# Optimization experiments

Hardware: AMD Instinct MI355X
Metric: run time of the kernel (lower is better)

The kernel has to match this reference:

```python
import jax, jax.numpy as jnp
import numpy as np

NUM_CLASSES = 14
IGNORE = 0
MAX_SAMPLES = 28 * 50
MAX_VIEWS = 50
TEMP = 0.1
THRESH = 0.3


def setup_inputs() -> dict:
    key = jax.random.key(0)
    B, Fd, D, H, W = 2, 128, 16, 128, 128
    N = B * D * H * W
    feats = jax.random.normal(key, (B, Fd, D, H, W), jnp.float32)
    idx = np.arange(N)
    pred = (idx % NUM_CLASSES).astype(np.int32)
    # alternate blocks: easy (label==pred) / hard (label!=pred) so every class
    # has >max_views pixels with >= n_view/2 hard and easy samples
    block = (idx // NUM_CLASSES) % 2
    lab = np.where(block == 0, pred, (pred + 1) % NUM_CLASSES).astype(np.int32)
    labels = jnp.asarray(lab.reshape(B, D, H, W))
    predict = jnp.asarray(pred.reshape(B, D, H, W))
    probability = jnp.ones((B, D, H, W), jnp.float32)
    queue = jax.random.normal(jax.random.fold_in(key, 1), (NUM_CLASSES, 4096, Fd), jnp.float32)
    return {"feats": feats, "labels": labels, "predict": predict,
            "probability": probability, "queue": queue}


def _l2n(x):
    return x / jnp.linalg.norm(x, axis=-1, keepdims=True)


def reference(feats, labels, predict, probability, queue):
    Fd = feats.shape[1]
    # [B, Fd, D, H, W] -> [N, Fd]
    f = jnp.transpose(feats, (0, 2, 3, 4, 1)).reshape(-1, Fd)
    lab = labels.reshape(-1)
    pred = predict.reshape(-1)
    valid = probability.reshape(-1) > THRESH
    N = f.shape[0]

    total_classes = NUM_CLASSES - 1              # all non-ignore classes qualify by construction
    n_view = min(MAX_SAMPLES // total_classes, MAX_VIEWS)  # = 50
    n_hard = n_view // 2                          # balanced branch always taken
    n_easy = n_view - n_hard
    idxs = jnp.arange(N)

    def pick(mask, k):
        # deterministic stand-in for randperm: first k valid indices
        keys = jnp.where(mask, idxs, N)
        return jnp.sort(keys)[:k]

    def sample_class(c):
        hard = valid & (pred == c) & (lab != c)
        easy = valid & (pred == c) & (lab == c)
        sel = jnp.concatenate([pick(hard, n_hard), pick(easy, n_easy)])
        return f[sel]

    classes = jnp.arange(1, NUM_CLASSES)
    X_ = jax.vmap(sample_class)(classes)          # [C-1, n_view, Fd]

    # positive queue: per-class mean of (threshold-filtered) feats
    onehot = jax.nn.one_hot(lab, NUM_CLASSES, dtype=f.dtype) * valid[:, None].astype(f.dtype)
    sums = jnp.einsum('nc,nd->cd', onehot, f)     # [C, Fd]
    cnts = onehot.sum(0)[:, None]
    pos_queue = sums / cnts                        # [C, Fd]

    # negatives: second half of cache, classes 1..C-1 (class 0 skipped in _sample_negative)
    neg = queue[1:, queue.shape[1] // 2:, :]       # [C-1, M, Fd]

    a = _l2n(X_)                                   # [C-1, V, Fd]
    p = _l2n(pos_queue[1:])                        # [C-1, Fd]
    n = _l2n(neg)                                  # [C-1, M, Fd]

    logits = jnp.einsum('cvd,cd->cv', a, p) / TEMP           # [C-1, V]
    neg_sum = jnp.exp(jnp.einsum('cvd,cmd->cvm', a, n) / TEMP).sum(-1)  # [C-1, V]
    log_prob = -logits + jnp.log(jnp.exp(logits) + neg_sum)
    # sum over classes of per-class mean, divided by num classes
    return log_prob.mean(axis=1).mean()
```

## Files before the change

### kernel.cpp

```cpp
#include <hip/hip_runtime.h>

#define NUMC 14
#define FD 128
#define SPATIAL (16*128*128)
#define N_TOTAL (2*SPATIAL)
#define NV 50
#define NH 25
#define TC 13
#define QLEN 4096
#define MCH 32
#define NCHUNK 64
#define NSTR (FD + 4)
#define NNEGBLK (TC * NCHUNK)
#define THRESH_F 0.3f

#define PXB 32768
#define CHB (SPATIAL / PXB)
#define NSUMBLK (256 * CHB)
#define NPI 64
#define GRPSZ 45
#define NGRP 64

typedef float f32x4 __attribute__((ext_vector_type(4)));

#define WS_LOSSP   0
#define WS_CNT0    16
#define WS_NEGPART 32
#define WS_ANORM   41632
#define WS_AROWS   42304
#define WS_PART    125504
#define WS_LAB8    240192

__global__ __launch_bounds__(256) void k_pre(const int* __restrict__ labels,
        const int* __restrict__ predict, const float* __restrict__ prob,
        const float* __restrict__ feats, unsigned char* __restrict__ lab8,
        float* __restrict__ arows, float* __restrict__ anorm, int* __restrict__ cnt0) {
    int blk = blockIdx.x;
    int tid = threadIdx.x;
    if (blk < 512) {
        int n = blk * 1024 + tid * 4;
        int4   lb = *(const int4*)(labels + n);
        float4 pv = *(const float4*)(prob + n);
        uchar4 o;
        o.x = pv.x > THRESH_F ? (unsigned char)((lb.x & 15) << 2) : (unsigned char)60;
        o.y = pv.y > THRESH_F ? (unsigned char)((lb.y & 15) << 2) : (unsigned char)60;
        o.z = pv.z > THRESH_F ? (unsigned char)((lb.z & 15) << 2) : (unsigned char)60;
        o.w = pv.w > THRESH_F ? (unsigned char)((lb.w & 15) << 2) : (unsigned char)60;
        *(uchar4*)(lab8 + n) = o;
        if (blk == 0 && tid == 0) cnt0[0] = 0;
    } else {
        __shared__ unsigned long long masks[4];
        __shared__ int n_tgt;
        __shared__ float red[2];
        int r = blk - 512;
        int ci = r / NV;
        int j  = r % NV;
        bool hard = j < NH;
        int target = hard ? j : j - NH;
        int c = ci + 1;
        if (tid == 0) n_tgt = N_TOTAL - 1;
        __syncthreads();
        int lane = tid & 63, w = tid >> 6;
        int found = 0;
        for (int base = 0; base < N_TOTAL && found <= target; base += 256) {
            int n = base + tid;
            int pr = predict[n];
            int lb = labels[n];
            float pb = prob[n];
            bool m = (pr == c) && (pb > THRESH_F) && (hard ? (lb != c) : (lb == c));
            unsigned long long mk = __ballot(m);
            if (lane == 0) masks[w] = mk;
            __syncthreads();
            int pre = 0;
            #pragma unroll
            for (int q = 0; q < 4; ++q)
                if (q < w) pre += __popcll(masks[q]);
            int rank = found + pre + __popcll(mk & ((1ull << lane) - 1ull));
            if (m && rank == target) n_tgt = n;
            found += __popcll(masks[0]) + __popcll(masks[1])
                   + __popcll(masks[2]) + __popcll(masks[3]);
            __syncthreads();
        }
        int n = n_tgt;
        if (tid < 128) {
            int b = n >> 18, sp = n & (SPATIAL - 1);
            float v = feats[((size_t)(b * FD + tid)) * SPATIAL + sp];
            arows[r * FD + tid] = v;
            float a = v * v;
            #pragma unroll
            for (int o = 32; o; o >>= 1) a += __shfl_xor(a, o);
            if ((tid & 63) == 0) red[tid >> 6] = a;
        }
        __syncthreads();
        if (tid == 0) anorm[r] = sqrtf(red[0] + red[1]);
    }
}

#define ACC(v, u) do { \
    acc[(u).x << 6] += (v).x; \
    acc[(u).y << 6] += (v).y; \
    acc[(u).z << 6] += (v).z; \
    acc[(u).w << 6] += (v).w; \
} while (0)

__global__ __launch_bounds__(256) void k_main(const float* __restrict__ feats,
        const unsigned char* __restrict__ lab8, const float* __restrict__ queue,
        const float* __restrict__ arows, const float* __restrict__ anorm,
        float* __restrict__ part, float* __restrict__ negpart) {
    __shared__ float smem[4352];
    int tid = threadIdx.x;
    int lane = tid & 63, w = tid >> 6;
    int g = blockIdx.x / GRPSZ;
    int l = blockIdx.x % GRPSZ;

    if (l < 13) {
        int nb = g * 13 + l;
        int ci = nb >> 6;
        int chunk = nb & 63;
        float* n_s  = smem;
        float* an_s = smem + 4224;
        if (tid < NV) an_s[tid] = anorm[ci * NV + tid];
        const float4* qp4 = (const float4*)(queue
            + ((size_t)(ci + 1) * QLEN + (QLEN / 2) + chunk * MCH) * (size_t)FD);
        for (int i = tid; i < MCH * (FD / 4); i += 256) {
            int m = i >> 5, k4 = i & 31;
            ((float4*)(n_s + m * NSTR))[k4] = qp4[i];
        }
        __syncthreads();
        int half = lane >> 5, l32 = lane & 31;
        const float4* nrow = (const float4*)(n_s + l32 * NSTR);
        float sq = 0.f;
        #pragma unroll
        for (int k = 0; k < FD / 4; ++k) {
            float4 t = nrow[k];
            sq += t.x*t.x + t.y*t.y + t.z*t.z + t.w*t.w;
        }
        float inn = 10.f * rsqrtf(sq);
        float* np = negpart + (size_t)(ci * NV) * NCHUNK + chunk;
        const float4* abase = (const float4*)(arows + (size_t)(ci * NV) * FD);
        for (int v = w * 2 + half; v < NV; v += 8) {
            const float4* a4 = abase + v * (FD / 4);
            float dot = 0.f;
            #pragma unroll
            for (int k = 0; k < FD / 4; ++k) {
                float4 x = a4[k], y = nrow[k];
                dot += x.x*y.x + x.y*y.y + x.z*y.z + x.w*y.w;
            }
            float e = __expf(dot * inn / an_s[v]);
            #pragma unroll
            for (int o = 16; o; o >>= 1) e += __shfl_xor(e, o);
            if (l32 == 0) np[(size_t)v * NCHUNK] = e;
        }
    } else {
        int sb = g * 32 + (l - 13);
        int plane = sb >> 3;
        int chunk = sb & (CHB - 1);
        int b = plane >> 7;
        int ch = plane & 127;
        float* acc = smem + tid;
        #pragma unroll
        for (int c = 0; c < 16; ++c) acc[c << 8] = 0.f;

        const f32x4*  fp4 = (const f32x4*)(feats + (size_t)plane * SPATIAL) + (chunk << 13);
        const uchar4* lp4 = (const uchar4*)(lab8 + (size_t)b * SPATIAL) + (chunk << 13);
        int idx = (sb * 5) & 31;
        f32x4  v = fp4[(idx << 8) + tid];
        uchar4 u = lp4[(idx << 8) + tid];
        for (int ii = 0; ii < 31; ++ii) {
            int nidx = (idx + 1) & 31;
            f32x4  vn = fp4[(nidx << 8) + tid];
            uchar4 un = lp4[(nidx << 8) + tid];
            ACC(v, u);
            v = vn; u = un; idx = nidx;
        }
        ACC(v, u);

        int pi = b * 32 + chunk * 4 + w;
        #pragma unroll
        for (int c = 0; c < NUMC; ++c) {
            float x = acc[c << 8];
            #pragma unroll
            for (int o = 32; o; o >>= 1) x += __shfl_xor(x, o);
            if (lane == 0) part[((size_t)c * NPI + pi) * FD + ch] = x;
        }
    }
}

__global__ __launch_bounds__(256) void k_loss(const float* __restrict__ arows,
        const float* __restrict__ anorm, const float* __restrict__ part,
        const float* __restrict__ negpart, float* __restrict__ lossp,
        int* __restrict__ cnt0, float* __restrict__ out) {
    __shared__ float p_s[FD];
    __shared__ float red_s[2];
    __shared__ float lacc[8];
    int tid = threadIdx.x;
    int ci = blockIdx.x, c = ci + 1;
    if (tid < 128) {
        const float* pp = part + (size_t)c * NPI * FD + tid;
        float s = 0.f;
        #pragma unroll 16
        for (int k = 0; k < NPI; ++k) s += pp[(size_t)k * FD];
        p_s[tid] = s;
    }
    __syncthreads();
    if (tid < 128) {
        float q = p_s[tid] * p_s[tid];
        #pragma unroll
        for (int o = 32; o; o >>= 1) q += __shfl_xor(q, o);
        if ((tid & 63) == 0) red_s[tid >> 6] = q;
    }
    __syncthreads();
    float pninv10 = 10.f * rsqrtf(red_s[0] + red_s[1]);
    int grp = tid >> 5, l32 = tid & 31;
    float acc = 0.f;
    for (int r = grp; r < NV; r += 8) {
        int ar = ci * NV + r;
        const float4* a4 = (const float4*)(arows + (size_t)ar * FD);
        const float4* p4 = (const float4*)p_s;
        float4 x = a4[l32], y = p4[l32];
        float d = x.x*y.x + x.y*y.y + x.z*y.z + x.w*y.w;
        float ns = negpart[(size_t)ar * NCHUNK + l32]
                 + negpart[(size_t)ar * NCHUNK + 32 + l32];
        #pragma unroll
        for (int o = 16; o; o >>= 1) { d += __shfl_xor(d, o); ns += __shfl_xor(ns, o); }
        if (l32 == 0) {
            float logit = d * pninv10 / anorm[ar];
            acc += -logit + logf(__expf(logit) + ns);
        }
    }
    if (l32 == 0) lacc[grp] = acc;
    __syncthreads();
    if (tid == 0) {
        float s = 0.f;
        #pragma unroll
        for (int i = 0; i < 8; ++i) s += lacc[i];
        lossp[ci] = s;
        __threadfence();
        int t = atomicAdd(cnt0, 1);
        if (t == TC - 1) {
            __threadfence();
            float tot = 0.f;
            for (int i = 0; i < TC; ++i)
                tot += __hip_atomic_load(lossp + i, __ATOMIC_RELAXED, __HIP_MEMORY_SCOPE_AGENT);
            out[0] = tot * (1.f / (TC * NV));
        }
    }
}

extern "C" void kernel_launch(void* const* d_in, const int* in_sizes, int n_in,
                              void* d_out, int out_size, void* d_ws, size_t ws_size,
                              hipStream_t stream) {
    (void)in_sizes; (void)n_in; (void)out_size; (void)ws_size;
    const float* feats   = (const float*)d_in[0];
    const int*   labels  = (const int*)d_in[1];
    const int*   predict = (const int*)d_in[2];
    const float* prob    = (const float*)d_in[3];
    const float* queue   = (const float*)d_in[4];
    float* ws  = (float*)d_ws;
    float* out = (float*)d_out;

    float* lossp   = ws + WS_LOSSP;
    int*   cnt0    = (int*)(ws + WS_CNT0);
    float* negpart = ws + WS_NEGPART;
    float* anorm   = ws + WS_ANORM;
    float* arows   = ws + WS_AROWS;
    float* part    = ws + WS_PART;
    unsigned char* lab8 = (unsigned char*)(ws + WS_LAB8);

    k_pre  <<<512 + TC * NV, 256, 0, stream>>>(labels, predict, prob, feats,
                                               lab8, arows, anorm, cnt0);
    k_main <<<NGRP * GRPSZ, 256, 0, stream>>>(feats, lab8, queue, arows, anorm,
                                              part, negpart);
    k_loss <<<TC, 256, 0, stream>>>(arows, anorm, part, negpart, lossp, cnt0, out);
}
```

Before: 96.86 us.

## Use half-plane sum blocks with 4-deep load pipelining in class-sum pass

The per-class feature-sum blocks now each cover half a feature plane instead of a 32768-pixel chunk, which cuts the sum block count, the partial-sum count, and the work of the final reduction. The inner loop keeps four loads in flight, replacing the single-step prefetch and the rotated start index. Longer blocks mean fewer blocks to fill the GPU and drop the staggered start that spread memory accesses, but give more bytes in flight per block.

```diff
diff --git a/kernel.cpp b/kernel.cpp
--- a/kernel.cpp
+++ b/kernel.cpp
@@ -14,11 +14,11 @@
 #define NNEGBLK (TC * NCHUNK)
 #define THRESH_F 0.3f
 
-#define PXB 32768
-#define CHB (SPATIAL / PXB)
-#define NSUMBLK (256 * CHB)
-#define NPI 64
-#define GRPSZ 45
+#define NSUMBLK 512
+#define HP (SPATIAL / 2)
+#define ITERS (HP / 1024)
+#define NPI 16
+#define GRPSZ 21
 #define NGRP 64
 
 typedef float f32x4 __attribute__((ext_vector_type(4)));
@@ -29,7 +29,7 @@
 #define WS_ANORM   41632
 #define WS_AROWS   42304
 #define WS_PART    125504
-#define WS_LAB8    240192
+#define WS_LAB8    154176
 
 __global__ __launch_bounds__(256) void k_pre(const int* __restrict__ labels,
         const int* __restrict__ predict, const float* __restrict__ prob,
@@ -152,30 +152,40 @@
             if (l32 == 0) np[(size_t)v * NCHUNK] = e;
         }
     } else {
-        int sb = g * 32 + (l - 13);
-        int plane = sb >> 3;
-        int chunk = sb & (CHB - 1);
+        int sb = g * 8 + (l - 13);
+        int plane = sb >> 1;
+        int half = sb & 1;
         int b = plane >> 7;
         int ch = plane & 127;
         float* acc = smem + tid;
         #pragma unroll
         for (int c = 0; c < 16; ++c) acc[c << 8] = 0.f;
 
-        const f32x4*  fp4 = (const f32x4*)(feats + (size_t)plane * SPATIAL) + (chunk << 13);
-        const uchar4* lp4 = (const uchar4*)(lab8 + (size_t)b * SPATIAL) + (chunk << 13);
-        int idx = (sb * 5) & 31;
-        f32x4  v = fp4[(idx << 8) + tid];
-        uchar4 u = lp4[(idx << 8) + tid];
-        for (int ii = 0; ii < 31; ++ii) {
-            int nidx = (idx + 1) & 31;
-            f32x4  vn = fp4[(nidx << 8) + tid];
-            uchar4 un = lp4[(nidx << 8) + tid];
-            ACC(v, u);
-            v = vn; u = un; idx = nidx;
-        }
-        ACC(v, u);
-
-        int pi = b * 32 + chunk * 4 + w;
+        const f32x4*  fp4 = (const f32x4*)(feats + (size_t)plane * SPATIAL + half * HP);
+        const uchar4* lp4 = (const uchar4*)(lab8 + (size_t)b * SPATIAL + half * HP);
+        f32x4  v0 = fp4[tid],       v1 = fp4[tid + 256];
+        f32x4  v2 = fp4[tid + 512], v3 = fp4[tid + 768];
+        uchar4 u0 = lp4[tid],       u1 = lp4[tid + 256];
+        uchar4 u2 = lp4[tid + 512], u3 = lp4[tid + 768];
+        for (int i = 0; i < ITERS - 4; i += 4) {
+            f32x4  p0 = fp4[(i + 4) * 256 + tid];
+            uchar4 q0 = lp4[(i + 4) * 256 + tid];
+            ACC(v0, u0);
+            f32x4  p1 = fp4[(i + 5) * 256 + tid];
+            uchar4 q1 = lp4[(i + 5) * 256 + tid];
+            ACC(v1, u1);
+            f32x4  p2 = fp4[(i + 6) * 256 + tid];
+            uchar4 q2 = lp4[(i + 6) * 256 + tid];
+            ACC(v2, u2);
+            f32x4  p3 = fp4[(i + 7) * 256 + tid];
+            uchar4 q3 = lp4[(i + 7) * 256 + tid];
+            ACC(v3, u3);
+            v0 = p0; u0 = q0; v1 = p1; u1 = q1;
+            v2 = p2; u2 = q2; v3 = p3; u3 = q3;
+        }
+        ACC(v0, u0); ACC(v1, u1); ACC(v2, u2); ACC(v3, u3);
+
+        int pi = (b * 2 + half) * 4 + w;
         #pragma unroll
         for (int c = 0; c < NUMC; ++c) {
             float x = acc[c << 8];
```

New measurement: 97.44 us. About the same (+0.6%).
